# Kernel optimization log

Measured on AMD Instinct MI355X. Metric: run time of the kernel, lower is better.

Reference implementation:

```python
import jax, jax.numpy as jnp
import numpy as np

N = 50000      # nodes
E = 800000     # edges (avg degree 16)
IN = 256       # in_dim == heads*hidden (so DGL residual is Identity)
H = 4          # heads
D = 64         # hidden_dim / out_dim per head
EPS = 1e-5
NEG_SLOPE_ATTN = 0.2   # DGL GATConv edge-attention leaky_relu slope
NEG_SLOPE_ACT = 0.01   # F.leaky_relu default


def gat_conv(x, src, dst, W, al, ar, b, act):
    # x: [N, H*D], W: [H*D, H*D], al/ar: [H, D], b: [H*D]
    feat = (x @ W).reshape(N, H, D)                       # [N,H,D]
    el = jnp.sum(feat * al, axis=-1)                      # [N,H]
    er = jnp.sum(feat * ar, axis=-1)                      # [N,H]
    e = jax.nn.leaky_relu(el[src] + er[dst], NEG_SLOPE_ATTN)  # [E,H]
    # segment softmax over incoming edges per destination node
    m = jax.ops.segment_max(e, dst, num_segments=N)       # [N,H]
    m = jnp.where(jnp.isfinite(m), m, 0.0)                # nodes with no in-edges
    ee = jnp.exp(e - m[dst])                              # [E,H]
    denom = jax.ops.segment_sum(ee, dst, num_segments=N)  # [N,H]
    alpha = ee / jnp.maximum(denom[dst], 1e-9)            # [E,H]
    msg = feat[src] * alpha[:, :, None]                   # [E,H,D]
    rst = jax.ops.segment_sum(msg, dst, num_segments=N)   # [N,H,D]
    rst = rst + x.reshape(N, H, D)                        # identity residual (dims match)
    rst = rst + b.reshape(1, H, D)
    if act:
        rst = jax.nn.leaky_relu(rst, NEG_SLOPE_ACT)
    return rst


def batch_norm(h, gamma, beta):
    # BatchNorm1d in training mode: batch statistics over node dim
    mu = jnp.mean(h, axis=0)
    var = jnp.var(h, axis=0)
    return (h - mu) * jax.lax.rsqrt(var + EPS) * gamma + beta


def setup_inputs():
    key = jax.random.key(0)
    ks = jax.random.split(key, 18)
    s = 1.0 / np.sqrt(IN)
    inp = {
        'x': jax.random.normal(ks[0], (N, IN), jnp.float32),
        'src': jax.random.randint(ks[1], (E,), 0, N),
        'dst': jax.random.randint(ks[2], (E,), 0, N),
    }
    names = ['W1', 'al1', 'ar1', 'b1', 'W2', 'al2', 'ar2', 'b2', 'W3', 'al3', 'ar3', 'b3']
    shapes = [(IN, H * D), (H, D), (H, D), (H * D,)] * 3
    for i, (nm, sh) in enumerate(zip(names, shapes)):
        inp[nm] = jax.random.normal(ks[3 + i], sh, jnp.float32) * s
    inp['g1'] = jnp.ones((H * D,), jnp.float32)
    inp['be1'] = jnp.zeros((H * D,), jnp.float32)
    inp['g2'] = jnp.ones((H * D,), jnp.float32)
    inp['be2'] = jnp.zeros((H * D,), jnp.float32)
    return inp


def reference(x, src, dst, W1, al1, ar1, b1, W2, al2, ar2, b2, W3, al3, ar3, b3, g1, be1, g2, be2):
    h = gat_conv(x, src, dst, W1, al1, ar1, b1, act=True).reshape(N, H * D)
    h = batch_norm(h, g1, be1)
    h = gat_conv(h, src, dst, W2, al2, ar2, b2, act=True).reshape(N, H * D)
    h = batch_norm(h, g2, be2)
    h = gat_conv(h, src, dst, W3, al3, ar3, b3, act=False)   # [N,H,D]
    return h.mean(axis=1)                                    # [N,D]
```

## Files before the change

kernel.cpp:

```cpp
#include <hip/hip_runtime.h>

constexpr int NN = 50000;
constexpr int NE = 800000;
constexpr float SLOPE_A = 0.2f;
constexpr float SLOPE_R = 0.01f;
constexpr int SCB = 196;

typedef __attribute__((ext_vector_type(8))) short bf16x8;
typedef __attribute__((ext_vector_type(4))) float f32x4;

__device__ __forceinline__ unsigned short f2bf(float f) {
    union { float f; unsigned u; } v; v.f = f;
    unsigned u = v.u;
    unsigned r = u + 0x7fffu + ((u >> 16) & 1u);
    return (unsigned short)(r >> 16);
}
__device__ __forceinline__ float bf2f(unsigned short s) {
    union { unsigned u; float f; } v; v.u = ((unsigned)s) << 16;
    return v.f;
}

__global__ void k_hist(const int* __restrict__ dst, int* __restrict__ cnt) {
    int i = blockIdx.x * 256 + threadIdx.x;
    if (i < NE) atomicAdd(&cnt[dst[i]], 1);
}

__global__ void k_scan1(const int* __restrict__ cnt, int* __restrict__ loc,
                        int* __restrict__ bsum) {
    __shared__ int sh[256];
    int t = threadIdx.x;
    int i = blockIdx.x * 256 + t;
    int v = (i < NN) ? cnt[i] : 0;
    sh[t] = v;
    __syncthreads();
    for (int off = 1; off < 256; off <<= 1) {
        int tmp = (t >= off) ? sh[t - off] : 0;
        __syncthreads();
        sh[t] += tmp;
        __syncthreads();
    }
    loc[i] = sh[t] - v;
    if (t == 255) bsum[blockIdx.x] = sh[255];
}

__global__ void k_scan2(const int* __restrict__ bsum, int* __restrict__ boff,
                        int* __restrict__ rowptr) {
    __shared__ int sh[256];
    int t = threadIdx.x;
    int v = (t < SCB) ? bsum[t] : 0;
    sh[t] = v;
    __syncthreads();
    for (int off = 1; off < 256; off <<= 1) {
        int tmp = (t >= off) ? sh[t - off] : 0;
        __syncthreads();
        sh[t] += tmp;
        __syncthreads();
    }
    if (t < SCB) boff[t] = sh[t] - v;
    if (t == 255) rowptr[NN] = sh[255];
}

__global__ void k_scan3(const int* __restrict__ loc, const int* __restrict__ boff,
                        int* __restrict__ rowptr, int* __restrict__ cursor) {
    int i = blockIdx.x * 256 + threadIdx.x;
    if (i < NN) {
        int r = loc[i] + boff[blockIdx.x];
        rowptr[i] = r;
        cursor[i] = r;
    }
}

__global__ void k_scatter(const int* __restrict__ src, const int* __restrict__ dst,
                          int* __restrict__ cursor, int* __restrict__ ssrc) {
    int i = blockIdx.x * 256 + threadIdx.x;
    if (i < NE) {
        int d = dst[i];
        int pos = atomicAdd(&cursor[d], 1);
        ssrc[pos] = src[i];
    }
}

__global__ void k_prepw(const float* __restrict__ W1, const float* __restrict__ W2,
                        const float* __restrict__ W3, unsigned short* __restrict__ Wt) {
    int b = blockIdx.x;
    int L = b >> 8, k = b & 255;
    const float* W = (L == 0) ? W1 : ((L == 1) ? W2 : W3);
    int j = threadIdx.x;
    Wt[L * 65536 + j * 256 + k] = f2bf(W[k * 256 + j]);
}

__global__ void k_fold(const unsigned short* __restrict__ Wt, const float* __restrict__ sc,
                       const float* __restrict__ sh, unsigned short* __restrict__ Wfrag,
                       float* __restrict__ cvec) {
    int b = blockIdx.x;
    if (b < 32) {
        int gid = b * 256 + threadIdx.x;
        int lane = gid & 63;
        int frag = gid >> 6;
        int j = frag & 3, kc = (frag >> 2) & 7, w = frag >> 5;
        int mm = lane & 15, q = lane >> 4;
        int n = 64 * w + 16 * j + mm;
        int k0 = kc * 32 + q * 8;
        const unsigned short* srcp = Wt + n * 256 + k0;
        unsigned short o[8];
        if (sc) {
#pragma unroll
            for (int t = 0; t < 8; t++)
                o[t] = f2bf(sc[k0 + t] * bf2f(srcp[t]));
        } else {
#pragma unroll
            for (int t = 0; t < 8; t++) o[t] = srcp[t];
        }
        *(uint4*)(Wfrag + (size_t)gid * 8) = *(const uint4*)o;
    } else {
        __shared__ float red[256];
        int n = b - 32;
        int k = threadIdx.x;
        red[k] = sh[k] * bf2f(Wt[n * 256 + k]);
        __syncthreads();
        for (int off = 128; off > 0; off >>= 1) {
            if (k < off) red[k] += red[k + off];
            __syncthreads();
        }
        if (k == 0) cvec[n] = red[0];
    }
}

__global__ void k_foldlr(const unsigned short* __restrict__ Wt, const float* __restrict__ sc,
                         const float* __restrict__ cvec, const float* __restrict__ al,
                         const float* __restrict__ ar, unsigned short* __restrict__ wlrfrag,
                         float* __restrict__ offlr) {
    __shared__ float lw[256][8];
    int k = threadIdx.x;
    float scv = sc ? sc[k] : 1.f;
    for (int h = 0; h < 4; h++) {
        float sl = 0.f, sr = 0.f;
        for (int d = 0; d < 64; d++) {
            float wv = bf2f(Wt[(64 * h + d) * 256 + k]);
            sl += wv * al[h * 64 + d];
            sr += wv * ar[h * 64 + d];
        }
        lw[k][2 * h] = scv * sl;
        lw[k][2 * h + 1] = scv * sr;
    }
    __syncthreads();
    int kc = k >> 5, rem = k & 31, q = rem >> 3, t = rem & 7;
    for (int mm = 0; mm < 16; mm++) {
        unsigned short v = 0;
        if (mm < 8) v = f2bf(lw[k][mm]);
        wlrfrag[kc * 512 + (q * 16 + mm) * 8 + t] = v;
    }
    if (k < 8) {
        float o = 0.f;
        if (cvec) {
            int h = k >> 1;
            const float* a = (k & 1) ? ar : al;
            for (int d = 0; d < 64; d++) o += cvec[64 * h + d] * a[h * 64 + d];
        }
        offlr[k] = o;
    }
}

__launch_bounds__(256, 2)
__global__ void k_gemm(const void* __restrict__ Araw, int af32,
                       const unsigned short* __restrict__ Wfrag,
                       const float* __restrict__ cvec,
                       const unsigned short* __restrict__ wlrfrag,
                       const float* __restrict__ offlr,
                       unsigned short* __restrict__ feat16, float* __restrict__ el,
                       float* __restrict__ er) {
    constexpr int AP = 264;
    __shared__ __align__(16) unsigned short Alds[64 * AP];
    const int tid = threadIdx.x;
    const int rowbase = blockIdx.x * 64;

    if (af32) {
        const float* A = (const float*)Araw;
        int r = tid >> 6;
        int c4 = tid & 63;
        for (int it = 0; it < 16; it++) {
            int rr = it * 4 + r;
            int gr = rowbase + rr;
            float4 v = make_float4(0.f, 0.f, 0.f, 0.f);
            if (gr < NN) v = *(const float4*)(A + (size_t)gr * 256 + c4 * 4);
            ushort4 pv;
            pv.x = f2bf(v.x); pv.y = f2bf(v.y); pv.z = f2bf(v.z); pv.w = f2bf(v.w);
            *(ushort4*)(&Alds[rr * AP + c4 * 4]) = pv;
        }
    } else {
        const unsigned short* A = (const unsigned short*)Araw;
        for (int it = 0; it < 8; it++) {
            int idx = it * 256 + tid;
            int rr = idx >> 5;
            int c16 = idx & 31;
            int gr = rowbase + rr;
            uint4 v = make_uint4(0u, 0u, 0u, 0u);
            if (gr < NN) v = *(const uint4*)(A + (size_t)gr * 256 + c16 * 8);
            *(uint4*)(&Alds[rr * AP + c16 * 8]) = v;
        }
    }
    __syncthreads();

    f32x4 acc[4][4];
    for (int i = 0; i < 4; i++)
        for (int j = 0; j < 4; j++)
            acc[i][j] = (f32x4){0.f, 0.f, 0.f, 0.f};
    f32x4 accLR[4];
    for (int i = 0; i < 4; i++) accLR[i] = (f32x4){0.f, 0.f, 0.f, 0.f};

    const int lane = tid & 63, w = tid >> 6;
    const int mm = lane & 15, q = lane >> 4;

    const unsigned short* bbase = Wfrag + ((size_t)w * 8 * 4) * 512 + (size_t)lane * 8;

#pragma unroll
    for (int kc = 0; kc < 8; kc++) {
        bf16x8 a[4], b[4];
        for (int i = 0; i < 4; i++)
            a[i] = *(const bf16x8*)(&Alds[(16 * i + mm) * AP + kc * 32 + q * 8]);
        for (int j = 0; j < 4; j++)
            b[j] = *(const bf16x8*)(bbase + (size_t)(kc * 4 + j) * 512);
        for (int i = 0; i < 4; i++)
            for (int j = 0; j < 4; j++)
                acc[i][j] = __builtin_amdgcn_mfma_f32_16x16x32_bf16(a[i], b[j], acc[i][j], 0, 0, 0);
        if (w == 0) {
            bf16x8 blr = *(const bf16x8*)(wlrfrag + kc * 512 + lane * 8);
            for (int i = 0; i < 4; i++)
                accLR[i] = __builtin_amdgcn_mfma_f32_16x16x32_bf16(a[i], blr, accLR[i], 0, 0, 0);
        }
    }
    __syncthreads();

    if (cvec) {
        float cv[4];
        for (int j = 0; j < 4; j++) cv[j] = cvec[64 * w + 16 * j + mm];
        for (int i = 0; i < 4; i++)
            for (int j = 0; j < 4; j++)
                for (int r = 0; r < 4; r++)
                    acc[i][j][r] += cv[j];
    }

    if (w == 0 && mm < 8) {
        float off = offlr[mm];
        int h = mm >> 1;
        float* dstp = (mm & 1) ? er : el;
        for (int i = 0; i < 4; i++)
            for (int r = 0; r < 4; r++) {
                int gr = rowbase + 16 * i + q * 4 + r;
                if (gr < NN) dstp[gr * 4 + h] = accLR[i][r] + off;
            }
    }

    for (int i = 0; i < 4; i++)
        for (int j = 0; j < 4; j++) {
            int gc = 64 * w + 16 * j + mm;
            for (int r = 0; r < 4; r++) {
                int rr = 16 * i + q * 4 + r;
                Alds[rr * AP + gc] = f2bf(acc[i][j][r]);
            }
        }
    __syncthreads();
    for (int it = 0; it < 8; it++) {
        int idx = it * 256 + tid;
        int rr = idx >> 5;
        int c16 = idx & 31;
        int gr = rowbase + rr;
        if (gr < NN)
            *(uint4*)(feat16 + (size_t)gr * 256 + c16 * 8) = *(const uint4*)(&Alds[rr * AP + c16 * 8]);
    }
}

__launch_bounds__(256)
__global__ void k_agg(const unsigned short* __restrict__ feat16, const float* __restrict__ el,
                      const float* __restrict__ er, const int* __restrict__ rowptr,
                      const int* __restrict__ ssrc,
                      const unsigned short* __restrict__ residh, const float* __restrict__ residf,
                      const float* __restrict__ bnscale, const float* __restrict__ bnshift,
                      int use_bn, const float* __restrict__ bias, int act,
                      unsigned short* __restrict__ outh, float* __restrict__ outf,
                      int final_mean) {
    int n = __builtin_amdgcn_readfirstlane(blockIdx.x * 4 + (threadIdx.x >> 6));
    int l = threadIdx.x & 63;
    int h = l >> 4;
    int beg = rowptr[n], end = rowptr[n + 1];
    float erh = er[n * 4 + h];

    float d = 0.f;
    float4 acc = make_float4(0.f, 0.f, 0.f, 0.f);

    for (int e = beg; e < end; e += 8) {
        int ss[8];
        float cc[8];
        ushort4 ff[8];
#pragma unroll
        for (int j = 0; j < 8; j++) {
            int ee = e + j;
            ss[j] = ssrc[(ee < end) ? ee : beg];
        }
#pragma unroll
        for (int j = 0; j < 8; j++)
            cc[j] = el[ss[j] * 4 + h];
#pragma unroll
        for (int j = 0; j < 8; j++)
            ff[j] = *(const ushort4*)(feat16 + (size_t)ss[j] * 256 + l * 4);
#pragma unroll
        for (int j = 0; j < 8; j++) {
            float sc = cc[j] + erh;
            sc = (sc > 0.f) ? sc : SLOPE_A * sc;
            float wgt = ((e + j) < end) ? __expf(sc) : 0.f;
            d += wgt;
            acc.x += bf2f(ff[j].x) * wgt;
            acc.y += bf2f(ff[j].y) * wgt;
            acc.z += bf2f(ff[j].z) * wgt;
            acc.w += bf2f(ff[j].w) * wgt;
        }
    }

    float invd = 1.f / fmaxf(d, 1e-9f);
    acc.x *= invd; acc.y *= invd; acc.z *= invd; acc.w *= invd;

    float4 r;
    if (residf) {
        r = *(const float4*)(residf + (size_t)n * 256 + l * 4);
    } else {
        ushort4 rv = *(const ushort4*)(residh + (size_t)n * 256 + l * 4);
        r = make_float4(bf2f(rv.x), bf2f(rv.y), bf2f(rv.z), bf2f(rv.w));
    }
    if (use_bn) {
        float4 sc4 = *(const float4*)(bnscale + l * 4);
        float4 sh4 = *(const float4*)(bnshift + l * 4);
        r.x = r.x * sc4.x + sh4.x;
        r.y = r.y * sc4.y + sh4.y;
        r.z = r.z * sc4.z + sh4.z;
        r.w = r.w * sc4.w + sh4.w;
    }
    float4 bb = *(const float4*)(bias + l * 4);
    acc.x += r.x + bb.x; acc.y += r.y + bb.y;
    acc.z += r.z + bb.z; acc.w += r.w + bb.w;
    if (act) {
        acc.x = (acc.x > 0.f) ? acc.x : SLOPE_R * acc.x;
        acc.y = (acc.y > 0.f) ? acc.y : SLOPE_R * acc.y;
        acc.z = (acc.z > 0.f) ? acc.z : SLOPE_R * acc.z;
        acc.w = (acc.w > 0.f) ? acc.w : SLOPE_R * acc.w;
    }

    if (!final_mean) {
        ushort4 p;
        p.x = f2bf(acc.x); p.y = f2bf(acc.y); p.z = f2bf(acc.z); p.w = f2bf(acc.w);
        *(ushort4*)(outh + (size_t)n * 256 + l * 4) = p;
    } else {
        acc.x += __shfl_xor(acc.x, 16, 64); acc.x += __shfl_xor(acc.x, 32, 64);
        acc.y += __shfl_xor(acc.y, 16, 64); acc.y += __shfl_xor(acc.y, 32, 64);
        acc.z += __shfl_xor(acc.z, 16, 64); acc.z += __shfl_xor(acc.z, 32, 64);
        acc.w += __shfl_xor(acc.w, 16, 64); acc.w += __shfl_xor(acc.w, 32, 64);
        if (l < 16) {
            acc.x *= 0.25f; acc.y *= 0.25f; acc.z *= 0.25f; acc.w *= 0.25f;
            *(float4*)(outf + (size_t)n * 64 + l * 4) = acc;
        }
    }
}

__global__ void k_bnstats(const unsigned short* __restrict__ hh, float* __restrict__ pbuf) {
    __shared__ float ps[8 * 256];
    __shared__ float ps2[8 * 256];
    int t = threadIdx.x, b = blockIdx.x;
    int r8 = t >> 5, c32 = t & 31;
    int r0 = b * 196, r1 = min(r0 + 196, NN);
    float s[8], s2[8];
#pragma unroll
    for (int e = 0; e < 8; e++) { s[e] = 0.f; s2[e] = 0.f; }
    for (int r = r0 + r8; r < r1; r += 8) {
        uint4 v = *(const uint4*)(hh + (size_t)r * 256 + c32 * 8);
        const unsigned short* pv = (const unsigned short*)&v;
#pragma unroll
        for (int e = 0; e < 8; e++) {
            float f = bf2f(pv[e]);
            s[e] += f; s2[e] += f * f;
        }
    }
#pragma unroll
    for (int e = 0; e < 8; e++) {
        ps[r8 * 256 + c32 * 8 + e] = s[e];
        ps2[r8 * 256 + c32 * 8 + e] = s2[e];
    }
    __syncthreads();
    float ts = 0.f, ts2 = 0.f;
    for (int g = 0; g < 8; g++) { ts += ps[g * 256 + t]; ts2 += ps2[g * 256 + t]; }
    pbuf[b * 512 + t] = ts;
    pbuf[b * 512 + 256 + t] = ts2;
}

__global__ void k_bnfinal(const float* __restrict__ pbuf, const float* __restrict__ g,
                          const float* __restrict__ be, float* __restrict__ scale,
                          float* __restrict__ shift) {
    int t = threadIdx.x;
    float s = 0.f, s2 = 0.f;
    for (int b = 0; b < 256; b++) {
        s += pbuf[b * 512 + t];
        s2 += pbuf[b * 512 + 256 + t];
    }
    float mu = s * (1.f / NN);
    float var = s2 * (1.f / NN) - mu * mu;
    float rs = rsqrtf(var + 1e-5f);
    float sc = rs * g[t];
    scale[t] = sc;
    shift[t] = be[t] - mu * sc;
}

extern "C" void kernel_launch(void* const* d_in, const int* in_sizes, int n_in,
                              void* d_out, int out_size, void* d_ws, size_t ws_size,
                              hipStream_t stream) {
    const float* x   = (const float*)d_in[0];
    const int* src   = (const int*)d_in[1];
    const int* dst   = (const int*)d_in[2];
    const float* W1  = (const float*)d_in[3];
    const float* al1 = (const float*)d_in[4];
    const float* ar1 = (const float*)d_in[5];
    const float* b1  = (const float*)d_in[6];
    const float* W2  = (const float*)d_in[7];
    const float* al2 = (const float*)d_in[8];
    const float* ar2 = (const float*)d_in[9];
    const float* b2  = (const float*)d_in[10];
    const float* W3  = (const float*)d_in[11];
    const float* al3 = (const float*)d_in[12];
    const float* ar3 = (const float*)d_in[13];
    const float* b3  = (const float*)d_in[14];
    const float* g1  = (const float*)d_in[15];
    const float* be1 = (const float*)d_in[16];
    const float* g2  = (const float*)d_in[17];
    const float* be2 = (const float*)d_in[18];
    float* out = (float*)d_out;

    char* ws = (char*)d_ws;
    size_t off = 0;
    auto alloc = [&](size_t bytes) {
        void* p = ws + off;
        off += (bytes + 255) & ~(size_t)255;
        return p;
    };
    int* rowptr = (int*)alloc((NN + 1) * sizeof(int));
    int* cursor = (int*)alloc(NN * sizeof(int));
    int* cnt    = (int*)alloc(SCB * 256 * sizeof(int));
    int* loc    = (int*)alloc(SCB * 256 * sizeof(int));
    int* bsum   = (int*)alloc(SCB * sizeof(int));
    int* boff   = (int*)alloc(SCB * sizeof(int));
    int* ssrc   = (int*)alloc(NE * sizeof(int));
    unsigned short* feat16 = (unsigned short*)alloc((size_t)NN * 256 * sizeof(unsigned short));
    unsigned short* hbuf   = (unsigned short*)alloc((size_t)NN * 256 * sizeof(unsigned short));
    float* el   = (float*)alloc((size_t)NN * 4 * sizeof(float));
    float* er   = (float*)alloc((size_t)NN * 4 * sizeof(float));
    unsigned short* Wt      = (unsigned short*)alloc(3 * 65536 * sizeof(unsigned short));
    unsigned short* Wfrag1  = (unsigned short*)alloc(65536 * sizeof(unsigned short));
    unsigned short* Wfrag2  = (unsigned short*)alloc(65536 * sizeof(unsigned short));
    unsigned short* wlrfrag = (unsigned short*)alloc(4096 * sizeof(unsigned short));
    float* offlr   = (float*)alloc(16 * sizeof(float));
    float* cvec    = (float*)alloc(256 * sizeof(float));
    float* pbuf    = (float*)alloc(256 * 512 * sizeof(float));
    float* bnscale = (float*)alloc(256 * sizeof(float));
    float* bnshift = (float*)alloc(256 * sizeof(float));

    hipMemsetAsync(cnt, 0, NN * sizeof(int), stream);
    k_hist<<<(NE + 255) / 256, 256, 0, stream>>>(dst, cnt);
    k_scan1<<<SCB, 256, 0, stream>>>(cnt, loc, bsum);
    k_scan2<<<1, 256, 0, stream>>>(bsum, boff, rowptr);
    k_scan3<<<SCB, 256, 0, stream>>>(loc, boff, rowptr, cursor);
    k_scatter<<<(NE + 255) / 256, 256, 0, stream>>>(src, dst, cursor, ssrc);
    k_prepw<<<768, 256, 0, stream>>>(W1, W2, W3, Wt);
    k_fold<<<32, 256, 0, stream>>>(Wt, nullptr, nullptr, Wfrag1, nullptr);
    k_foldlr<<<1, 256, 0, stream>>>(Wt, nullptr, nullptr, al1, ar1, wlrfrag, offlr);

    const int GB = (NN + 63) / 64;
    const int NB = NN / 4;

    k_gemm<<<GB, 256, 0, stream>>>(x, 1, Wfrag1, nullptr, wlrfrag, offlr, feat16, el, er);
    k_agg<<<NB, 256, 0, stream>>>(feat16, el, er, rowptr, ssrc, nullptr, x,
                                  nullptr, nullptr, 0, b1, 1, hbuf, nullptr, 0);
    k_bnstats<<<256, 256, 0, stream>>>(hbuf, pbuf);
    k_bnfinal<<<1, 256, 0, stream>>>(pbuf, g1, be1, bnscale, bnshift);
    k_fold<<<288, 256, 0, stream>>>(Wt + 65536, bnscale, bnshift, Wfrag2, cvec);
    k_foldlr<<<1, 256, 0, stream>>>(Wt + 65536, bnscale, cvec, al2, ar2, wlrfrag, offlr);

    k_gemm<<<GB, 256, 0, stream>>>(hbuf, 0, Wfrag2, cvec, wlrfrag, offlr, feat16, el, er);
    k_agg<<<NB, 256, 0, stream>>>(feat16, el, er, rowptr, ssrc, hbuf, nullptr,
                                  bnscale, bnshift, 1, b2, 1, hbuf, nullptr, 0);
    k_bnstats<<<256, 256, 0, stream>>>(hbuf, pbuf);
    k_bnfinal<<<1, 256, 0, stream>>>(pbuf, g2, be2, bnscale, bnshift);
    k_fold<<<288, 256, 0, stream>>>(Wt + 131072, bnscale, bnshift, Wfrag2, cvec);
    k_foldlr<<<1, 256, 0, stream>>>(Wt + 131072, bnscale, cvec, al3, ar3, wlrfrag, offlr);

    k_gemm<<<GB, 256, 0, stream>>>(hbuf, 0, Wfrag2, cvec, wlrfrag, offlr, feat16, el, er);
    k_agg<<<NB, 256, 0, stream>>>(feat16, el, er, rowptr, ssrc, hbuf, nullptr,
                                  bnscale, bnshift, 1, b3, 0, nullptr, out, 1);
}
```

Baseline: 577.2 us.

## Fuse weight prep into fold kernel and widen aggregation edge batch to 16

Removes the separate bf16 transpose kernel and the single-block attention-vector fold kernel. The fold kernel now reads fp32 weights directly and computes the el/er projection columns in 8 extra blocks, with the offsets computed in parallel (one block per head/side). This cuts launches and replaces a serial single-block kernel. The aggregation loop also gathers 16 edges per iteration instead of 8, exposing more memory-level parallelism at the cost of more registers and more wasted lanes on low-degree nodes.

```diff
diff --git a/kernel.cpp b/kernel.cpp
--- a/kernel.cpp
+++ b/kernel.cpp
@@ -80,18 +80,11 @@
     }
 }
 
-__global__ void k_prepw(const float* __restrict__ W1, const float* __restrict__ W2,
-                        const float* __restrict__ W3, unsigned short* __restrict__ Wt) {
-    int b = blockIdx.x;
-    int L = b >> 8, k = b & 255;
-    const float* W = (L == 0) ? W1 : ((L == 1) ? W2 : W3);
-    int j = threadIdx.x;
-    Wt[L * 65536 + j * 256 + k] = f2bf(W[k * 256 + j]);
-}
-
-__global__ void k_fold(const unsigned short* __restrict__ Wt, const float* __restrict__ sc,
-                       const float* __restrict__ sh, unsigned short* __restrict__ Wfrag,
-                       float* __restrict__ cvec) {
+__global__ void k_fold(const float* __restrict__ W, const float* __restrict__ sc,
+                       const float* __restrict__ sh, const float* __restrict__ al,
+                       const float* __restrict__ ar, unsigned short* __restrict__ Wfrag,
+                       float* __restrict__ cvec, unsigned short* __restrict__ wlrfrag,
+                       float* __restrict__ offlr, int has_bn) {
     int b = blockIdx.x;
     if (b < 32) {
         int gid = b * 256 + threadIdx.x;
@@ -101,63 +94,45 @@
         int mm = lane & 15, q = lane >> 4;
         int n = 64 * w + 16 * j + mm;
         int k0 = kc * 32 + q * 8;
-        const unsigned short* srcp = Wt + n * 256 + k0;
         unsigned short o[8];
-        if (sc) {
-#pragma unroll
-            for (int t = 0; t < 8; t++)
-                o[t] = f2bf(sc[k0 + t] * bf2f(srcp[t]));
-        } else {
-#pragma unroll
-            for (int t = 0; t < 8; t++) o[t] = srcp[t];
+#pragma unroll
+        for (int t = 0; t < 8; t++) {
+            float wv = W[(size_t)(k0 + t) * 256 + n];
+            if (sc) wv *= sc[k0 + t];
+            o[t] = f2bf(wv);
         }
         *(uint4*)(Wfrag + (size_t)gid * 8) = *(const uint4*)o;
-    } else {
+    } else if (has_bn && b < 288) {
         __shared__ float red[256];
-        int n = b - 32;
-        int k = threadIdx.x;
-        red[k] = sh[k] * bf2f(Wt[n * 256 + k]);
+        int n = b - 32, k = threadIdx.x;
+        red[k] = sh[k] * W[(size_t)k * 256 + n];
         __syncthreads();
         for (int off = 128; off > 0; off >>= 1) {
             if (k < off) red[k] += red[k + off];
             __syncthreads();
         }
         if (k == 0) cvec[n] = red[0];
-    }
-}
-
-__global__ void k_foldlr(const unsigned short* __restrict__ Wt, const float* __restrict__ sc,
-                         const float* __restrict__ cvec, const float* __restrict__ al,
-                         const float* __restrict__ ar, unsigned short* __restrict__ wlrfrag,
-                         float* __restrict__ offlr) {
-    __shared__ float lw[256][8];
-    int k = threadIdx.x;
-    float scv = sc ? sc[k] : 1.f;
-    for (int h = 0; h < 4; h++) {
-        float sl = 0.f, sr = 0.f;
-        for (int d = 0; d < 64; d++) {
-            float wv = bf2f(Wt[(64 * h + d) * 256 + k]);
-            sl += wv * al[h * 64 + d];
-            sr += wv * ar[h * 64 + d];
-        }
-        lw[k][2 * h] = scv * sl;
-        lw[k][2 * h + 1] = scv * sr;
-    }
-    __syncthreads();
-    int kc = k >> 5, rem = k & 31, q = rem >> 3, t = rem & 7;
-    for (int mm = 0; mm < 16; mm++) {
-        unsigned short v = 0;
-        if (mm < 8) v = f2bf(lw[k][mm]);
-        wlrfrag[kc * 512 + (q * 16 + mm) * 8 + t] = v;
-    }
-    if (k < 8) {
-        float o = 0.f;
-        if (cvec) {
-            int h = k >> 1;
-            const float* a = (k & 1) ? ar : al;
-            for (int d = 0; d < 64; d++) o += cvec[64 * h + d] * a[h * 64 + d];
-        }
-        offlr[k] = o;
+    } else {
+        int n = b - (has_bn ? 288 : 32);
+        int h = n >> 1;
+        const float* a = (n & 1) ? ar : al;
+        int k = threadIdx.x;
+        float raw = 0.f;
+#pragma unroll 8
+        for (int d = 0; d < 64; d++)
+            raw += W[(size_t)k * 256 + 64 * h + d] * a[h * 64 + d];
+        float val = (sc ? sc[k] : 1.f) * raw;
+        int kc = k >> 5, rem = k & 31, q = rem >> 3, t = rem & 7;
+        wlrfrag[kc * 512 + (q * 16 + n) * 8 + t] = f2bf(val);
+        wlrfrag[kc * 512 + (q * 16 + n + 8) * 8 + t] = 0;
+        __shared__ float red[256];
+        red[k] = sh ? sh[k] * raw : 0.f;
+        __syncthreads();
+        for (int off = 128; off > 0; off >>= 1) {
+            if (k < off) red[k] += red[k + off];
+            __syncthreads();
+        }
+        if (k == 0) offlr[n] = red[0];
     }
 }
 
@@ -288,23 +263,23 @@
     float d = 0.f;
     float4 acc = make_float4(0.f, 0.f, 0.f, 0.f);
 
-    for (int e = beg; e < end; e += 8) {
-        int ss[8];
-        float cc[8];
-        ushort4 ff[8];
-#pragma unroll
-        for (int j = 0; j < 8; j++) {
+    for (int e = beg; e < end; e += 16) {
+        int ss[16];
+        float cc[16];
+        ushort4 ff[16];
+#pragma unroll
+        for (int j = 0; j < 16; j++) {
             int ee = e + j;
             ss[j] = ssrc[(ee < end) ? ee : beg];
         }
 #pragma unroll
-        for (int j = 0; j < 8; j++)
+        for (int j = 0; j < 16; j++)
             cc[j] = el[ss[j] * 4 + h];
 #pragma unroll
-        for (int j = 0; j < 8; j++)
+        for (int j = 0; j < 16; j++)
             ff[j] = *(const ushort4*)(feat16 + (size_t)ss[j] * 256 + l * 4);
 #pragma unroll
-        for (int j = 0; j < 8; j++) {
+        for (int j = 0; j < 16; j++) {
             float sc = cc[j] + erh;
             sc = (sc > 0.f) ? sc : SLOPE_A * sc;
             float wgt = ((e + j) < end) ? __expf(sc) : 0.f;
@@ -449,7 +424,6 @@
     unsigned short* hbuf   = (unsigned short*)alloc((size_t)NN * 256 * sizeof(unsigned short));
     float* el   = (float*)alloc((size_t)NN * 4 * sizeof(float));
     float* er   = (float*)alloc((size_t)NN * 4 * sizeof(float));
-    unsigned short* Wt      = (unsigned short*)alloc(3 * 65536 * sizeof(unsigned short));
     unsigned short* Wfrag1  = (unsigned short*)alloc(65536 * sizeof(unsigned short));
     unsigned short* Wfrag2  = (unsigned short*)alloc(65536 * sizeof(unsigned short));
     unsigned short* wlrfrag = (unsigned short*)alloc(4096 * sizeof(unsigned short));
@@ -465,9 +439,8 @@
     k_scan2<<<1, 256, 0, stream>>>(bsum, boff, rowptr);
     k_scan3<<<SCB, 256, 0, stream>>>(loc, boff, rowptr, cursor);
     k_scatter<<<(NE + 255) / 256, 256, 0, stream>>>(src, dst, cursor, ssrc);
-    k_prepw<<<768, 256, 0, stream>>>(W1, W2, W3, Wt);
-    k_fold<<<32, 256, 0, stream>>>(Wt, nullptr, nullptr, Wfrag1, nullptr);
-    k_foldlr<<<1, 256, 0, stream>>>(Wt, nullptr, nullptr, al1, ar1, wlrfrag, offlr);
+    k_fold<<<40, 256, 0, stream>>>(W1, nullptr, nullptr, al1, ar1,
+                                   Wfrag1, nullptr, wlrfrag, offlr, 0);
 
     const int GB = (NN + 63) / 64;
     const int NB = NN / 4;
@@ -477,16 +450,16 @@
                                   nullptr, nullptr, 0, b1, 1, hbuf, nullptr, 0);
     k_bnstats<<<256, 256, 0, stream>>>(hbuf, pbuf);
     k_bnfinal<<<1, 256, 0, stream>>>(pbuf, g1, be1, bnscale, bnshift);
-    k_fold<<<288, 256, 0, stream>>>(Wt + 65536, bnscale, bnshift, Wfrag2, cvec);
-    k_foldlr<<<1, 256, 0, stream>>>(Wt + 65536, bnscale, cvec, al2, ar2, wlrfrag, offlr);
+    k_fold<<<296, 256, 0, stream>>>(W2, bnscale, bnshift, al2, ar2,
+                                    Wfrag2, cvec, wlrfrag, offlr, 1);
 
     k_gemm<<<GB, 256, 0, stream>>>(hbuf, 0, Wfrag2, cvec, wlrfrag, offlr, feat16, el, er);
     k_agg<<<NB, 256, 0, stream>>>(feat16, el, er, rowptr, ssrc, hbuf, nullptr,
                                   bnscale, bnshift, 1, b2, 1, hbuf, nullptr, 0);
     k_bnstats<<<256, 256, 0, stream>>>(hbuf, pbuf);
     k_bnfinal<<<1, 256, 0, stream>>>(pbuf, g2, be2, bnscale, bnshift);
-    k_fold<<<288, 256, 0, stream>>>(Wt + 131072, bnscale, bnshift, Wfrag2, cvec);
-    k_foldlr<<<1, 256, 0, stream>>>(Wt + 131072, bnscale, cvec, al3, ar3, wlrfrag, offlr);
+    k_fold<<<296, 256, 0, stream>>>(W3, bnscale, bnshift, al3, ar3,
+                                    Wfrag2, cvec, wlrfrag, offlr, 1);
 
     k_gemm<<<GB, 256, 0, stream>>>(hbuf, 0, Wfrag2, cvec, wlrfrag, offlr, feat16, el, er);
     k_agg<<<NB, 256, 0, stream>>>(feat16, el, er, rowptr, ssrc, hbuf, nullptr,
```

Measured after the change: 554.3 us. -4.0%, faster.
